# Performance work log

Measured on AMD Instinct MI355X. Metric: run time of the kernel, lower is better.

The kernel has to match this reference:

```python
import jax, jax.numpy as jnp
from jax import lax
import numpy as np

IMG_H = 14; IMG_W = 14
L = 21   # num_labels
M = 5    # num_mixture_filters
KL = 50  # local conv kernel
PL = 25  # local conv padding
HO = IMG_H + 2 * PL - KL + 1  # 15, locally-connected output size
CH = [(64, 3), (64, 64), (128, 64), (128, 128), (256, 128), (256, 256), (256, 256),
      (512, 256), (512, 512), (512, 512), (512, 512), (512, 512), (512, 512)]
DIL = [1, 1, 1, 1, 1, 1, 1, 1, 1, 1, 2, 2, 2]


def setup_inputs() -> dict:
    keys = iter(jax.random.split(jax.random.key(0), 80))
    def rnd(shape, s=0.05):
        return jax.random.normal(next(keys), shape, dtype=jnp.float32) * s
    d = {"x": jax.random.normal(next(keys), (2, 3, IMG_H, IMG_W), dtype=jnp.float32)}
    for i, (o, c) in enumerate(CH):
        d["w%d" % (i + 1)] = rnd((o, c, 3, 3))
        d["b%d" % (i + 1)] = rnd((o,))
    d["wf1"] = rnd((4096, 512, 7, 7), s=0.01); d["bf1"] = rnd((4096,))
    d["wf2"] = rnd((4096, 4096, 1, 1), s=0.01); d["bf2"] = rnd((4096,))
    d["wf3"] = rnd((L, 4096, 1, 1), s=0.01); d["bf3"] = rnd((L,))
    d["wl"] = rnd((HO, HO, L, L, KL, KL), s=0.01)  # per-position local-conv weights
    d["bl"] = rnd((L, HO, HO))
    d["wa"] = rnd((L, L)); d["ba"] = rnd((L,))
    d["wm"] = rnd((L * M, L, 9, 9, L)); d["bm"] = rnd((L * M,))
    d["wb"] = rnd((L * M, L * M)); d["bb"] = rnd((L * M,))
    return d


def _conv2d(x, w, b, pad, dil=1):
    y = lax.conv_general_dilated(x, w, (1, 1), [(pad, pad), (pad, pad)],
                                 rhs_dilation=(dil, dil),
                                 dimension_numbers=("NCHW", "OIHW", "NCHW"))
    return y + b[None, :, None, None]


def _maxpool2(x):
    return lax.reduce_window(x, -jnp.inf, lax.max, (1, 1, 2, 2), (1, 1, 2, 2), "VALID")


def _upsample_bilinear_ac(x, H, W):
    # UpsamplingBilinear2d == bilinear with align_corners=True
    def lerp(t, n_in, n_out, axis):
        src = jnp.arange(n_out, dtype=jnp.float32) * (float(n_in - 1) / max(n_out - 1, 1))
        i0 = jnp.clip(jnp.floor(src).astype(jnp.int32), 0, max(n_in - 2, 0))
        i1 = jnp.minimum(i0 + 1, n_in - 1)
        f = src - i0.astype(jnp.float32)
        shp = [1] * t.ndim; shp[axis] = n_out
        f = f.reshape(shp).astype(t.dtype)
        return jnp.take(t, i0, axis=axis) * (1 - f) + jnp.take(t, i1, axis=axis) * f
    return lerp(lerp(x, x.shape[2], H, 2), x.shape[3], W, 3)


def reference(x, w1, b1, w2, b2, w3, b3, w4, b4, w5, b5, w6, b6, w7, b7, w8, b8,
              w9, b9, w10, b10, w11, b11, w12, b12, w13, b13,
              wf1, bf1, wf2, bf2, wf3, bf3, wl, bl, wa, ba, wm, bm, wb, bb):
    ws = [w1, w2, w3, w4, w5, w6, w7, w8, w9, w10, w11, w12, w13]
    bs = [b1, b2, b3, b4, b5, b6, b7, b8, b9, b10, b11, b12, b13]
    h = x
    for i in range(13):
        h = jax.nn.relu(_conv2d(h, ws[i], bs[i], pad=DIL[i], dil=DIL[i]))
        if i in (1, 3, 6):  # MaxPool2d after VGG blocks 1,2,3
            h = _maxpool2(h)
    h = jax.nn.relu(_conv2d(h, wf1, bf1, pad=12, dil=4))  # 7x7 dilated FC-conv
    h = jax.nn.relu(_conv2d(h, wf2, bf2, pad=0))
    h = _conv2d(h, wf3, bf3, pad=0)                       # -> [B, L, h', w']
    h = jax.nn.sigmoid(_upsample_bilinear_ac(h, IMG_H, IMG_W))
    # Conv2dLocal: locally-connected 50x50 conv, per-position weights
    xp = jnp.pad(h, ((0, 0), (0, 0), (PL, PL), (PL, PL)))
    idx = jnp.arange(HO)[:, None] + jnp.arange(KL)[None, :]  # [HO, KL]
    p = xp[:, :, idx, :][:, :, :, :, idx]  # [B, C, HO, KL, HO, KL]
    h = jnp.einsum("bcisjt,ijocst->boij", p, wl) + bl[None]  # [B, L, HO, HO]
    # Linear over the label (channel) axis
    h = jnp.einsum("bchw,oc->bohw", h, wa) + ba[None, :, None, None]
    # Conv3d mixture head: label axis unsqueezed to depth-1 last spatial dim,
    # kernel (9, 9, L) with padding (4, 4, L//2) -> depth out = 1
    y = lax.conv_general_dilated(h[..., None], wm, (1, 1, 1),
                                 [(4, 4), (4, 4), (L // 2, L // 2)],
                                 dimension_numbers=("NCDHW", "OIDHW", "NCDHW"))
    h = y[..., 0] + bm[None, :, None, None]  # [B, L*M, HO, HO]
    h = jnp.einsum("bchw,oc->bohw", h, wb) + bb[None, :, None, None]
    # BlockMinPooling(kernel=M) over last dim: split into (M, W//M), min over block axis
    B_, C_, H_, W_ = h.shape
    h = h.reshape(B_, C_, H_, M, W_ // M).min(axis=3)  # [B, L*M, HO, HO//M]
    # AvgPool2d(kernel=1, stride=1, divisor_override=1) is the identity
    return jax.nn.softmax(h, axis=1)
```

## Files before the change

### kernel.cpp

```cpp
#include <hip/hip_runtime.h>
#include <math.h>

#define HO 15
#define LBL 21
#define MIX 5
#define LM 105
#define NB 256
#define NT 512
#define GSZ (NB * NT)
#define NWV (GSZ / 64)

struct Params {
    const float* x;
    const float* w[14]; const float* b[14];
    const float *wf1, *bf1, *wf2, *bf2, *wf3, *bf3;
    const float *wl, *bl, *wa, *ba, *wm, *bm, *wb, *bb;
    float *A, *B, *v, *h1, *h3, *out;
    int* bar;
};

__device__ __forceinline__ float max4(float a, float b, float c, float d) {
    return fmaxf(fmaxf(a, b), fmaxf(c, d));
}

__device__ __forceinline__ void gbar(int* bar, int id) {
    __syncthreads();
    if (threadIdx.x == 0) {
        __threadfence();
        int* c = bar + id * 16;
        __hip_atomic_fetch_add(c, 1, __ATOMIC_RELAXED, __HIP_MEMORY_SCOPE_AGENT);
        while (__hip_atomic_load(c, __ATOMIC_RELAXED, __HIP_MEMORY_SCOPE_AGENT) < NB)
            __builtin_amdgcn_s_sleep(16);
        (void)__hip_atomic_load(c, __ATOMIC_ACQUIRE, __HIP_MEMORY_SCOPE_AGENT);
    }
    __syncthreads();
}

template <int Cin, int Cout, int Hi, int H, int POOL>
__device__ void wconv(const float* __restrict__ in, const float* __restrict__ w,
                      const float* __restrict__ bias, float* __restrict__ out,
                      int gw, int lane) {
    constexpr int CPL = Cin / 64;
    for (int idx = gw; idx < 2 * Cout * H * H; idx += NWV) {
        int x = idx % H; int t = idx / H;
        int y = t % H; t /= H;
        int o = t % Cout; int b = t / Cout;
        const float* ip = in + (size_t)b * Cin * Hi * Hi;
        float acc = 0.f;
#pragma unroll
        for (int cc = 0; cc < CPL; ++cc) {
            int c = lane + 64 * cc;
            const float* ic = ip + (size_t)c * Hi * Hi;
            const float* wc = w + ((size_t)o * Cin + c) * 9;
#pragma unroll
            for (int ky = 0; ky < 3; ++ky) {
                int yy = y + ky - 1;
                if (yy < 0 || yy >= H) continue;
#pragma unroll
                for (int kx = 0; kx < 3; ++kx) {
                    int xx = x + kx - 1;
                    if (xx < 0 || xx >= H) continue;
                    float val;
                    if (POOL == 1) {
                        val = ic[yy * Hi + xx];
                    } else {
                        const float* q = ic + (2 * yy) * Hi + 2 * xx;
                        val = max4(q[0], q[1], q[Hi], q[Hi + 1]);
                    }
                    acc += val * wc[ky * 3 + kx];
                }
            }
        }
#pragma unroll
        for (int off = 32; off; off >>= 1) acc += __shfl_xor(acc, off);
        if (lane == 0) out[idx] = fmaxf(acc + bias[o], 0.f);
    }
}

template <int Cin, int ACT, int POOLIN>
__device__ void mvtap(const float* __restrict__ in, const float* __restrict__ w,
                      const float* __restrict__ bias, float* __restrict__ out,
                      int Cout, int S, int F, float* sin, int tid, int gw, int lane) {
    if (POOLIN) {
        for (int c = tid; c < 2 * Cin; c += NT) {
            const float* q = in + (size_t)c * 9;
            sin[c] = max4(q[0], q[1], q[3], q[4]);
        }
    } else {
        for (int c = tid; c < 2 * Cin; c += NT) sin[c] = in[c];
    }
    __syncthreads();
    constexpr int K = Cin / 64;
    int step = (Cout < NWV) ? (NWV / Cout) : 1;
    for (int u = gw; u < Cout * step; u += NWV) {
        if (step > 1 && (u % step) != 0) continue;
        int o = u / step;
        if (o >= Cout) continue;
        const float* wp = w + ((size_t)o * Cin + lane) * S + F;
        float a0 = 0.f, a1 = 0.f;
#pragma unroll
        for (int k = 0; k < K; ++k) {
            float i0 = sin[lane + 64 * k];
            float i1 = sin[Cin + lane + 64 * k];
            float wv = 0.f;
            if (i0 != 0.f || i1 != 0.f)
                wv = wp[(size_t)(64 * S) * k];
            a0 += wv * i0;
            a1 += wv * i1;
        }
#pragma unroll
        for (int off = 32; off; off >>= 1) {
            a0 += __shfl_xor(a0, off);
            a1 += __shfl_xor(a1, off);
        }
        if (lane == 0) {
            float bv = bias[o];
            a0 += bv; a1 += bv;
            if (ACT == 1) { a0 = fmaxf(a0, 0.f); a1 = fmaxf(a1, 0.f); }
            if (ACT == 2) { a0 = 1.f / (1.f + expf(-a0)); a1 = 1.f / (1.f + expf(-a1)); }
            out[o] = a0;
            out[Cout + o] = a1;
        }
    }
}

template <int Cin, int ACT>
__device__ void mvrow4(const float* __restrict__ in, const float* __restrict__ w,
                       const float* __restrict__ bias, float* __restrict__ out,
                       int Cout, float* sin, int tid, int gw, int lane) {
    for (int c = tid; c < 2 * Cin; c += NT) sin[c] = in[c];
    __syncthreads();
    constexpr int K4 = Cin / 256;
    const float4* s0 = (const float4*)sin;
    const float4* s1 = (const float4*)(sin + Cin);
    int step = (Cout < NWV) ? (NWV / Cout) : 1;
    for (int u = gw; u < Cout * step; u += NWV) {
        if (step > 1 && (u % step) != 0) continue;
        int o = u / step;
        if (o >= Cout) continue;
        const float4* wp = (const float4*)(w + (size_t)o * Cin) + lane;
        float a0 = 0.f, a1 = 0.f;
#pragma unroll
        for (int k = 0; k < K4; ++k) {
            float4 wv = wp[64 * k];
            float4 xv = s0[lane + 64 * k];
            float4 yv = s1[lane + 64 * k];
            a0 += wv.x * xv.x + wv.y * xv.y + wv.z * xv.z + wv.w * xv.w;
            a1 += wv.x * yv.x + wv.y * yv.y + wv.z * yv.z + wv.w * yv.w;
        }
#pragma unroll
        for (int off = 32; off; off >>= 1) {
            a0 += __shfl_xor(a0, off);
            a1 += __shfl_xor(a1, off);
        }
        if (lane == 0) {
            float bv = bias[o];
            a0 += bv; a1 += bv;
            if (ACT == 1) { a0 = fmaxf(a0, 0.f); a1 = fmaxf(a1, 0.f); }
            if (ACT == 2) { a0 = 1.f / (1.f + expf(-a0)); a1 = 1.f / (1.f + expf(-a1)); }
            out[o] = a0;
            out[Cout + o] = a1;
        }
    }
}

__device__ void localstage(const float* __restrict__ wl, const float* __restrict__ bl,
                           const float* __restrict__ v, float* __restrict__ h1,
                           int gw, int lane) {
    int e1 = lane + 64, e2 = lane + 128, e3 = lane + 192;
    int off0 = (lane / 14) * 50 + lane % 14;
    int off1 = (e1 / 14) * 50 + e1 % 14;
    int off2 = (e2 / 14) * 50 + e2 % 14;
    int off3 = (lane < 4) ? ((e3 / 14) * 50 + e3 % 14) : off0;
    float m3 = (lane < 4) ? 1.f : 0.f;
    for (int wk = gw; wk < LBL * HO * HO; wk += NWV) {
        int j = wk % HO; int t1 = wk / HO;
        int i = t1 % HO; int o = t1 / HO;
        int s0 = 25 - i, t0 = 25 - j;
        size_t base_ij = ((size_t)(i * HO + j) * LBL + o) * LBL;
        const float* pij = wl + base_ij * 2500 + s0 * 50 + t0;
        float a0 = 0.f, a1 = 0.f;
#pragma unroll 7
        for (int c = 0; c < LBL; ++c) {
            const float* p = pij + (size_t)c * 2500;
            float part = p[off0] + p[off1] + p[off2] + m3 * p[off3];
            a0 += v[c] * part;
            a1 += v[LBL + c] * part;
        }
#pragma unroll
        for (int off = 32; off; off >>= 1) {
            a0 += __shfl_xor(a0, off);
            a1 += __shfl_xor(a1, off);
        }
        if (lane == 0) {
            float bv = bl[(o * HO + i) * HO + j];
            h1[(size_t)(0 * LBL + o) * 225 + i * HO + j] = a0 + bv;
            h1[(size_t)(1 * LBL + o) * 225 + i * HO + j] = a1 + bv;
        }
    }
}

__device__ void ninestage(const float* __restrict__ h1, const float* __restrict__ wa,
                          const float* __restrict__ ba, const float* __restrict__ wm,
                          const float* __restrict__ bm, float* __restrict__ h3,
                          float* smem, int tid) {
    int blk = blockIdx.x;
    if (blk >= 2 * LM) return;
    float* s1 = smem;
    float* s2 = smem + 4725;
    float* sw = smem + 9450;
    float* swa = smem + 11151;
    int b = blk / LM, o = blk % LM;
    for (int k = tid; k < 4725; k += NT) s1[k] = h1[(size_t)b * 4725 + k];
    for (int k = tid; k < 441; k += NT) swa[k] = wa[k];
    for (int k = tid; k < 1701; k += NT) sw[k] = wm[((size_t)o * 1701 + k) * LBL + 10];
    __syncthreads();
    for (int k = tid; k < 4725; k += NT) {
        int c = k / 225, pix = k % 225;
        float acc = ba[c];
#pragma unroll 7
        for (int c2 = 0; c2 < LBL; ++c2)
            acc += swa[c * LBL + c2] * s1[c2 * 225 + pix];
        s2[k] = acc;
    }
    __syncthreads();
    if (tid >= 225) return;
    int i = tid / HO, j = tid % HO;
    float acc = bm[o];
    for (int c = 0; c < LBL; ++c) {
        const float* wp = sw + c * 81;
        const float* hp = s2 + c * 225;
#pragma unroll
        for (int di = 0; di < 9; ++di) {
            int y = i + di - 4;
            if (y < 0 || y >= HO) continue;
#pragma unroll
            for (int dj = 0; dj < 9; ++dj) {
                int x = j + dj - 4;
                if (x < 0 || x >= HO) continue;
                acc += hp[y * HO + x] * wp[di * 9 + dj];
            }
        }
    }
    h3[((size_t)b * LM + o) * 225 + tid] = acc;
}

__device__ void finalstage(const float* __restrict__ h3, const float* __restrict__ wbw,
                           const float* __restrict__ bbv, float* __restrict__ out,
                           float* smem, int tid) {
    int blk = blockIdx.x;
    if (blk >= 2 * HO * 3) return;
    float* sv = smem;
    float* sred = smem + 112;
    int k = blk % 3; int t = blk / 3; int i = t % HO; int b = t / HO;
    int o = tid;
    if (o < LM) {
        float mn = 3.4e38f;
        for (int mm = 0; mm < MIX; ++mm) {
            int j = mm * 3 + k;
            float acc = bbv[o];
            const float* hp = h3 + (size_t)b * LM * 225 + i * HO + j;
            const float* wp = wbw + o * LM;
#pragma unroll 5
            for (int c = 0; c < LM; ++c) acc += wp[c] * hp[(size_t)c * 225];
            mn = fminf(mn, acc);
        }
        sv[o] = mn;
    }
    __syncthreads();
    if (tid < 64) {
        float m = -3.4e38f;
        for (int c = tid; c < LM; c += 64) m = fmaxf(m, sv[c]);
#pragma unroll
        for (int off = 32; off; off >>= 1) m = fmaxf(m, __shfl_xor(m, off));
        if (tid == 0) sred[0] = m;
    }
    __syncthreads();
    if (o < LM) sv[o] = expf(sv[o] - sred[0]);
    __syncthreads();
    if (tid < 64) {
        float s = 0.f;
        for (int c = tid; c < LM; c += 64) s += sv[c];
#pragma unroll
        for (int off = 32; off; off >>= 1) s += __shfl_xor(s, off);
        if (tid == 0) sred[1] = s;
    }
    __syncthreads();
    if (o < LM) out[(((size_t)b * LM + o) * HO + i) * 3 + k] = sv[o] / sred[1];
}

__global__ __launch_bounds__(NT, 1) void mega(Params p) {
    const int tid = threadIdx.x;
    const int gtid = blockIdx.x * NT + tid;
    const int gw = gtid >> 6;
    const int lane = tid & 63;
    __shared__ float smem[11592];

    for (int idx = gtid; idx < 2 * 64 * 196; idx += GSZ) {
        int x = idx % 14; int t = idx / 14;
        int y = t % 14; t /= 14;
        int o = t % 64; int b = t / 64;
        const float* ip = p.x + (size_t)b * 3 * 196;
        const float* wp = p.w[1] + (size_t)o * 27;
        float acc = p.b[1][o];
#pragma unroll
        for (int c = 0; c < 3; ++c) {
            const float* ic = ip + c * 196;
            const float* wc = wp + c * 9;
#pragma unroll
            for (int ky = 0; ky < 3; ++ky) {
                int yy = y + ky - 1;
                if (yy < 0 || yy >= 14) continue;
#pragma unroll
                for (int kx = 0; kx < 3; ++kx) {
                    int xx = x + kx - 1;
                    if (xx < 0 || xx >= 14) continue;
                    acc += ic[yy * 14 + xx] * wc[ky * 3 + kx];
                }
            }
        }
        p.A[idx] = fmaxf(acc, 0.f);
    }
    gbar(p.bar, 0);

    wconv<64,  64, 14, 14, 1>(p.A, p.w[2], p.b[2], p.B, gw, lane);  gbar(p.bar, 1);
    wconv<64, 128, 14,  7, 2>(p.B, p.w[3], p.b[3], p.A, gw, lane);  gbar(p.bar, 2);
    wconv<128,128,  7,  7, 1>(p.A, p.w[4], p.b[4], p.B, gw, lane);  gbar(p.bar, 3);
    wconv<128,256,  7,  3, 2>(p.B, p.w[5], p.b[5], p.A, gw, lane);  gbar(p.bar, 4);
    wconv<256,256,  3,  3, 1>(p.A, p.w[6], p.b[6], p.B, gw, lane);  gbar(p.bar, 5);
    wconv<256,256,  3,  3, 1>(p.B, p.w[7], p.b[7], p.A, gw, lane);  gbar(p.bar, 6);

    mvtap<256, 1, 1>(p.A, p.w[8],  p.b[8],  p.B, 512, 9, 4, smem, tid, gw, lane);   gbar(p.bar, 7);
    mvtap<512, 1, 0>(p.B, p.w[9],  p.b[9],  p.A, 512, 9, 4, smem, tid, gw, lane);   gbar(p.bar, 8);
    mvtap<512, 1, 0>(p.A, p.w[10], p.b[10], p.B, 512, 9, 4, smem, tid, gw, lane);   gbar(p.bar, 9);
    mvtap<512, 1, 0>(p.B, p.w[11], p.b[11], p.A, 512, 9, 4, smem, tid, gw, lane);   gbar(p.bar, 10);
    mvtap<512, 1, 0>(p.A, p.w[12], p.b[12], p.B, 512, 9, 4, smem, tid, gw, lane);   gbar(p.bar, 11);
    mvtap<512, 1, 0>(p.B, p.w[13], p.b[13], p.A, 512, 9, 4, smem, tid, gw, lane);   gbar(p.bar, 12);
    mvtap<512, 1, 0>(p.A, p.wf1, p.bf1, p.B, 4096, 49, 24, smem, tid, gw, lane);    gbar(p.bar, 13);
    mvrow4<4096, 1>(p.B, p.wf2, p.bf2, p.A, 4096, smem, tid, gw, lane);             gbar(p.bar, 14);
    mvrow4<4096, 2>(p.A, p.wf3, p.bf3, p.v, 21, smem, tid, gw, lane);               gbar(p.bar, 15);

    localstage(p.wl, p.bl, p.v, p.h1, gw, lane);                     gbar(p.bar, 16);
    ninestage(p.h1, p.wa, p.ba, p.wm, p.bm, p.h3, smem, tid);        gbar(p.bar, 17);
    finalstage(p.h3, p.wb, p.bb, p.out, smem, tid);
}

extern "C" void kernel_launch(void* const* d_in, const int* in_sizes, int n_in,
                              void* d_out, int out_size, void* d_ws, size_t ws_size,
                              hipStream_t stream) {
    Params p;
    p.x = (const float*)d_in[0];
    for (int i = 1; i <= 13; ++i) {
        p.w[i] = (const float*)d_in[2 * i - 1];
        p.b[i] = (const float*)d_in[2 * i];
    }
    p.wf1 = (const float*)d_in[27]; p.bf1 = (const float*)d_in[28];
    p.wf2 = (const float*)d_in[29]; p.bf2 = (const float*)d_in[30];
    p.wf3 = (const float*)d_in[31]; p.bf3 = (const float*)d_in[32];
    p.wl  = (const float*)d_in[33]; p.bl  = (const float*)d_in[34];
    p.wa  = (const float*)d_in[35]; p.ba  = (const float*)d_in[36];
    p.wm  = (const float*)d_in[37]; p.bm  = (const float*)d_in[38];
    p.wb  = (const float*)d_in[39]; p.bb  = (const float*)d_in[40];

    float* wsf = (float*)d_ws;
    p.bar = (int*)d_ws;
    p.A  = wsf + 1024;
    p.B  = wsf + 1024 + 32768;
    p.v  = wsf + 1024 + 65536;
    p.h1 = wsf + 1024 + 65600;
    p.h3 = wsf + 1024 + 75072;
    p.out = (float*)d_out;

    hipMemsetAsync(d_ws, 0, 4096, stream);
    hipLaunchKernelGGL(mega, dim3(NB), dim3(NT), 0, stream, p);
}
```

Before: 608.5 us.

## Precompute local-conv weight window sums in chunks overlapped with backbone stages

```diff
diff --git a/kernel.cpp b/kernel.cpp
--- a/kernel.cpp
+++ b/kernel.cpp
@@ -9,13 +9,15 @@
 #define NT 512
 #define GSZ (NB * NT)
 #define NWV (GSZ / 64)
+#define NTASK (LBL * HO * HO * LBL)
+#define CHUNK ((NTASK + 15) / 16)
 
 struct Params {
     const float* x;
     const float* w[14]; const float* b[14];
     const float *wf1, *bf1, *wf2, *bf2, *wf3, *bf3;
     const float *wl, *bl, *wa, *ba, *wm, *bm, *wb, *bb;
-    float *A, *B, *v, *h1, *h3, *out;
+    float *A, *B, *v, *h1, *h3, *WS, *out;
     int* bar;
 };
 
@@ -34,6 +36,29 @@
         (void)__hip_atomic_load(c, __ATOMIC_ACQUIRE, __HIP_MEMORY_SCOPE_AGENT);
     }
     __syncthreads();
+}
+
+__device__ void wsgather(const float* __restrict__ wl, float* __restrict__ WS,
+                         int ph, int gw, int lane) {
+    int lo = ph * CHUNK;
+    int hi = lo + CHUNK; if (hi > NTASK) hi = NTASK;
+    int e1 = lane + 64, e2 = lane + 128, e3 = lane + 192;
+    int off0 = (lane / 14) * 50 + lane % 14;
+    int off1 = (e1 / 14) * 50 + e1 % 14;
+    int off2 = (e2 / 14) * 50 + e2 % 14;
+    int off3 = (lane < 4) ? ((e3 / 14) * 50 + e3 % 14) : off0;
+    float m3 = (lane < 4) ? 1.f : 0.f;
+    for (int tk = lo + gw; tk < hi; tk += NWV) {
+        int c = tk % LBL; int wk = tk / LBL;
+        int j = wk % HO; int t1 = wk / HO;
+        int i = t1 % HO; int o = t1 / HO;
+        const float* p = wl + (((size_t)(i * HO + j) * LBL + o) * LBL + c) * 2500
+                           + (25 - i) * 50 + (25 - j);
+        float s = p[off0] + p[off1] + p[off2] + m3 * p[off3];
+#pragma unroll
+        for (int off = 32; off; off >>= 1) s += __shfl_xor(s, off);
+        if (lane == 0) WS[tk] = s;
+    }
 }
 
 template <int Cin, int Cout, int Hi, int H, int POOL>
@@ -164,39 +189,22 @@
     }
 }
 
-__device__ void localstage(const float* __restrict__ wl, const float* __restrict__ bl,
-                           const float* __restrict__ v, float* __restrict__ h1,
-                           int gw, int lane) {
-    int e1 = lane + 64, e2 = lane + 128, e3 = lane + 192;
-    int off0 = (lane / 14) * 50 + lane % 14;
-    int off1 = (e1 / 14) * 50 + e1 % 14;
-    int off2 = (e2 / 14) * 50 + e2 % 14;
-    int off3 = (lane < 4) ? ((e3 / 14) * 50 + e3 % 14) : off0;
-    float m3 = (lane < 4) ? 1.f : 0.f;
-    for (int wk = gw; wk < LBL * HO * HO; wk += NWV) {
+__device__ void localws(const float* __restrict__ WS, const float* __restrict__ bl,
+                        const float* __restrict__ v, float* __restrict__ h1, int gtid) {
+    for (int wk = gtid; wk < LBL * HO * HO; wk += GSZ) {
         int j = wk % HO; int t1 = wk / HO;
         int i = t1 % HO; int o = t1 / HO;
-        int s0 = 25 - i, t0 = 25 - j;
-        size_t base_ij = ((size_t)(i * HO + j) * LBL + o) * LBL;
-        const float* pij = wl + base_ij * 2500 + s0 * 50 + t0;
+        const float* wsp = WS + (size_t)wk * LBL;
         float a0 = 0.f, a1 = 0.f;
-#pragma unroll 7
+#pragma unroll
         for (int c = 0; c < LBL; ++c) {
-            const float* p = pij + (size_t)c * 2500;
-            float part = p[off0] + p[off1] + p[off2] + m3 * p[off3];
-            a0 += v[c] * part;
-            a1 += v[LBL + c] * part;
-        }
-#pragma unroll
-        for (int off = 32; off; off >>= 1) {
-            a0 += __shfl_xor(a0, off);
-            a1 += __shfl_xor(a1, off);
-        }
-        if (lane == 0) {
-            float bv = bl[(o * HO + i) * HO + j];
-            h1[(size_t)(0 * LBL + o) * 225 + i * HO + j] = a0 + bv;
-            h1[(size_t)(1 * LBL + o) * 225 + i * HO + j] = a1 + bv;
-        }
+            float s = wsp[c];
+            a0 += v[c] * s;
+            a1 += v[LBL + c] * s;
+        }
+        float bv = bl[(o * HO + i) * HO + j];
+        h1[(size_t)(0 * LBL + o) * 225 + i * HO + j] = a0 + bv;
+        h1[(size_t)(1 * LBL + o) * 225 + i * HO + j] = a1 + bv;
     }
 }
 
@@ -321,26 +329,27 @@
         }
         p.A[idx] = fmaxf(acc, 0.f);
     }
+    wsgather(p.wl, p.WS, 0, gw, lane);
     gbar(p.bar, 0);
 
-    wconv<64,  64, 14, 14, 1>(p.A, p.w[2], p.b[2], p.B, gw, lane);  gbar(p.bar, 1);
-    wconv<64, 128, 14,  7, 2>(p.B, p.w[3], p.b[3], p.A, gw, lane);  gbar(p.bar, 2);
-    wconv<128,128,  7,  7, 1>(p.A, p.w[4], p.b[4], p.B, gw, lane);  gbar(p.bar, 3);
-    wconv<128,256,  7,  3, 2>(p.B, p.w[5], p.b[5], p.A, gw, lane);  gbar(p.bar, 4);
-    wconv<256,256,  3,  3, 1>(p.A, p.w[6], p.b[6], p.B, gw, lane);  gbar(p.bar, 5);
-    wconv<256,256,  3,  3, 1>(p.B, p.w[7], p.b[7], p.A, gw, lane);  gbar(p.bar, 6);
-
-    mvtap<256, 1, 1>(p.A, p.w[8],  p.b[8],  p.B, 512, 9, 4, smem, tid, gw, lane);   gbar(p.bar, 7);
-    mvtap<512, 1, 0>(p.B, p.w[9],  p.b[9],  p.A, 512, 9, 4, smem, tid, gw, lane);   gbar(p.bar, 8);
-    mvtap<512, 1, 0>(p.A, p.w[10], p.b[10], p.B, 512, 9, 4, smem, tid, gw, lane);   gbar(p.bar, 9);
-    mvtap<512, 1, 0>(p.B, p.w[11], p.b[11], p.A, 512, 9, 4, smem, tid, gw, lane);   gbar(p.bar, 10);
-    mvtap<512, 1, 0>(p.A, p.w[12], p.b[12], p.B, 512, 9, 4, smem, tid, gw, lane);   gbar(p.bar, 11);
-    mvtap<512, 1, 0>(p.B, p.w[13], p.b[13], p.A, 512, 9, 4, smem, tid, gw, lane);   gbar(p.bar, 12);
-    mvtap<512, 1, 0>(p.A, p.wf1, p.bf1, p.B, 4096, 49, 24, smem, tid, gw, lane);    gbar(p.bar, 13);
-    mvrow4<4096, 1>(p.B, p.wf2, p.bf2, p.A, 4096, smem, tid, gw, lane);             gbar(p.bar, 14);
-    mvrow4<4096, 2>(p.A, p.wf3, p.bf3, p.v, 21, smem, tid, gw, lane);               gbar(p.bar, 15);
-
-    localstage(p.wl, p.bl, p.v, p.h1, gw, lane);                     gbar(p.bar, 16);
+    wconv<64,  64, 14, 14, 1>(p.A, p.w[2], p.b[2], p.B, gw, lane);  wsgather(p.wl, p.WS, 1, gw, lane); gbar(p.bar, 1);
+    wconv<64, 128, 14,  7, 2>(p.B, p.w[3], p.b[3], p.A, gw, lane);  wsgather(p.wl, p.WS, 2, gw, lane); gbar(p.bar, 2);
+    wconv<128,128,  7,  7, 1>(p.A, p.w[4], p.b[4], p.B, gw, lane);  wsgather(p.wl, p.WS, 3, gw, lane); gbar(p.bar, 3);
+    wconv<128,256,  7,  3, 2>(p.B, p.w[5], p.b[5], p.A, gw, lane);  wsgather(p.wl, p.WS, 4, gw, lane); gbar(p.bar, 4);
+    wconv<256,256,  3,  3, 1>(p.A, p.w[6], p.b[6], p.B, gw, lane);  wsgather(p.wl, p.WS, 5, gw, lane); gbar(p.bar, 5);
+    wconv<256,256,  3,  3, 1>(p.B, p.w[7], p.b[7], p.A, gw, lane);  wsgather(p.wl, p.WS, 6, gw, lane); gbar(p.bar, 6);
+
+    mvtap<256, 1, 1>(p.A, p.w[8],  p.b[8],  p.B, 512, 9, 4, smem, tid, gw, lane);  wsgather(p.wl, p.WS, 7, gw, lane);  gbar(p.bar, 7);
+    mvtap<512, 1, 0>(p.B, p.w[9],  p.b[9],  p.A, 512, 9, 4, smem, tid, gw, lane);  wsgather(p.wl, p.WS, 8, gw, lane);  gbar(p.bar, 8);
+    mvtap<512, 1, 0>(p.A, p.w[10], p.b[10], p.B, 512, 9, 4, smem, tid, gw, lane);  wsgather(p.wl, p.WS, 9, gw, lane);  gbar(p.bar, 9);
+    mvtap<512, 1, 0>(p.B, p.w[11], p.b[11], p.A, 512, 9, 4, smem, tid, gw, lane);  wsgather(p.wl, p.WS, 10, gw, lane); gbar(p.bar, 10);
+    mvtap<512, 1, 0>(p.A, p.w[12], p.b[12], p.B, 512, 9, 4, smem, tid, gw, lane);  wsgather(p.wl, p.WS, 11, gw, lane); gbar(p.bar, 11);
+    mvtap<512, 1, 0>(p.B, p.w[13], p.b[13], p.A, 512, 9, 4, smem, tid, gw, lane);  wsgather(p.wl, p.WS, 12, gw, lane); gbar(p.bar, 12);
+    mvtap<512, 1, 0>(p.A, p.wf1, p.bf1, p.B, 4096, 49, 24, smem, tid, gw, lane);   wsgather(p.wl, p.WS, 13, gw, lane); gbar(p.bar, 13);
+    mvrow4<4096, 1>(p.B, p.wf2, p.bf2, p.A, 4096, smem, tid, gw, lane);            wsgather(p.wl, p.WS, 14, gw, lane); gbar(p.bar, 14);
+    mvrow4<4096, 2>(p.A, p.wf3, p.bf3, p.v, 21, smem, tid, gw, lane);              wsgather(p.wl, p.WS, 15, gw, lane); gbar(p.bar, 15);
+
+    localws(p.WS, p.bl, p.v, p.h1, gtid);                            gbar(p.bar, 16);
     ninestage(p.h1, p.wa, p.ba, p.wm, p.bm, p.h3, smem, tid);        gbar(p.bar, 17);
     finalstage(p.h3, p.wb, p.bb, p.out, smem, tid);
 }
@@ -369,6 +378,7 @@
     p.v  = wsf + 1024 + 65536;
     p.h1 = wsf + 1024 + 65600;
     p.h3 = wsf + 1024 + 75072;
+    p.WS = wsf + 1024 + 122432;
     p.out = (float*)d_out;
 
     hipMemsetAsync(d_ws, 0, 4096, stream);
```

Result: slower. 663.5 us (+9.0%).
